# Optimization experiments

Hardware: AMD Instinct MI355X
Metric: run time of the kernel (lower is better)

## Reference

```python
import jax, jax.numpy as jnp
import numpy as np

B, H, W, C = 2, 256, 256, 96
NH, WS, SS = 3, 8, 4
HD = C // NH
N = WS * WS              # tokens per window
NWIMG = (H // WS) * (W // WS)  # windows per image
MLP = 4 * C
EPS = 1e-5

def _np_attn_mask():
    img = np.zeros((H, W))
    sl = (slice(0, -WS), slice(-WS, -SS), slice(-SS, None))
    cnt = 0
    for a in sl:
        for b in sl:
            img[a, b] = cnt
            cnt += 1
    m = img.reshape(H // WS, WS, W // WS, WS).transpose(0, 2, 1, 3).reshape(-1, N)
    am = m[:, None, :] - m[:, :, None]
    return np.where(am != 0, -100.0, 0.0).astype(np.float32)

def _np_rel_index():
    coords = np.stack(np.meshgrid(np.arange(WS), np.arange(WS), indexing='ij'))
    cf = coords.reshape(2, -1)
    rel = (cf[:, :, None] - cf[:, None, :]).transpose(1, 2, 0).copy()
    rel[..., 0] += WS - 1
    rel[..., 1] += WS - 1
    rel[..., 0] *= 2 * WS - 1
    return rel.sum(-1)

def _np_coords_table():
    r = np.arange(-(WS - 1), WS, dtype=np.float32)
    t = np.stack(np.meshgrid(r, r, indexing='ij'), axis=-1) / (WS - 1) * 8.0
    t = np.sign(t) * np.log2(np.abs(t) + 1.0) / np.log2(8.0)
    return t.reshape(-1, 2)

ATTN_MASK = jnp.asarray(_np_attn_mask())          # [NWIMG, N, N]
REL_INDEX = jnp.asarray(_np_rel_index().reshape(-1))
COORDS_TABLE = jnp.asarray(_np_coords_table())    # [(2WS-1)^2, 2]

def setup_inputs():
    key = jax.random.key(0)
    ks = jax.random.split(key, 16)
    s = 0.02
    return {
        'hidden_states': jax.random.normal(ks[0], (B, H * W, C), jnp.float32),
        'time': jax.random.uniform(ks[1], (B,), jnp.float32),
        'q_w': jax.random.normal(ks[2], (C, C), jnp.float32) * s,
        'q_b': jnp.zeros((C,), jnp.float32),
        'k_w': jax.random.normal(ks[3], (C, C), jnp.float32) * s,
        'v_w': jax.random.normal(ks[4], (C, C), jnp.float32) * s,
        'v_b': jnp.zeros((C,), jnp.float32),
        'proj_w': jax.random.normal(ks[5], (C, C), jnp.float32) * s,
        'proj_b': jnp.zeros((C,), jnp.float32),
        'logit_scale': jnp.full((NH, 1, 1), jnp.log(10.0), jnp.float32),
        'cpb_w1': jax.random.normal(ks[6], (2, 512), jnp.float32) * s,
        'cpb_b1': jnp.zeros((512,), jnp.float32),
        'cpb_w2': jax.random.normal(ks[7], (512, NH), jnp.float32) * s,
        'lnb_ww': jax.random.normal(ks[8], (1, C), jnp.float32) * s,
        'lnb_wb': jnp.ones((C,), jnp.float32),
        'lnb_bw': jax.random.normal(ks[9], (1, C), jnp.float32) * s,
        'lnb_bb': jnp.zeros((C,), jnp.float32),
        'lna_ww': jax.random.normal(ks[10], (1, C), jnp.float32) * s,
        'lna_wb': jnp.ones((C,), jnp.float32),
        'lna_bw': jax.random.normal(ks[11], (1, C), jnp.float32) * s,
        'lna_bb': jnp.zeros((C,), jnp.float32),
        'fc1_w': jax.random.normal(ks[12], (C, MLP), jnp.float32) * s,
        'fc1_b': jnp.zeros((MLP,), jnp.float32),
        'fc2_w': jax.random.normal(ks[13], (MLP, C), jnp.float32) * s,
        'fc2_b': jnp.zeros((C,), jnp.float32),
    }

def _cln(x, time, ww, wb, bw, bb):
    # ConditionalLayerNorm: stats over channels, affine params from time via Linear(1, C)
    mean = x.mean(-1, keepdims=True)
    var = (x * x).mean(-1, keepdims=True) - mean * mean
    xn = (x - mean) / jnp.sqrt(var + EPS)
    t = time.reshape(-1, 1)
    w = (t @ ww + wb)[:, None, :]
    b = (t @ bw + bb)[:, None, :]
    return w * xn + b

def reference(hidden_states, time, q_w, q_b, k_w, v_w, v_b, proj_w, proj_b, logit_scale, cpb_w1, cpb_b1, cpb_w2, lnb_ww, lnb_wb, lnb_bw, lnb_bb, lna_ww, lna_wb, lna_bw, lna_bb, fc1_w, fc1_b, fc2_w, fc2_b):
    shortcut = hidden_states
    x = hidden_states.reshape(B, H, W, C)
    x = jnp.roll(x, (-SS, -SS), axis=(1, 2))  # cyclic shift
    # window partition -> [nW, N, C]
    xw = x.reshape(B, H // WS, WS, W // WS, WS, C).transpose(0, 1, 3, 2, 4, 5).reshape(-1, N, C)
    nW = B * NWIMG
    q = (xw @ q_w + q_b).reshape(nW, N, NH, HD).transpose(0, 2, 1, 3)
    k = (xw @ k_w).reshape(nW, N, NH, HD).transpose(0, 2, 1, 3)  # key has no bias in Swinv2
    v = (xw @ v_w + v_b).reshape(nW, N, NH, HD).transpose(0, 2, 1, 3)
    # cosine attention with clamped learnable log temperature
    qn = q / jnp.maximum(jnp.linalg.norm(q, axis=-1, keepdims=True), 1e-12)
    kn = k / jnp.maximum(jnp.linalg.norm(k, axis=-1, keepdims=True), 1e-12)
    scale = jnp.exp(jnp.minimum(logit_scale, jnp.log(100.0)))  # [NH,1,1]
    attn = jnp.einsum('whnd,whmd->whnm', qn, kn) * scale[None]
    # continuous relative position bias: MLP(2->512->NH) over log-spaced coords
    bias_table = jax.nn.relu(COORDS_TABLE @ cpb_w1 + cpb_b1) @ cpb_w2
    bias = bias_table[REL_INDEX].reshape(N, N, NH).transpose(2, 0, 1)
    attn = attn + 16.0 * jax.nn.sigmoid(bias)[None]
    # shifted-window mask
    attn = attn.reshape(B, NWIMG, NH, N, N) + ATTN_MASK[None, :, None]
    attn = jax.nn.softmax(attn.reshape(nW, NH, N, N), axis=-1)
    ctx = jnp.einsum('whnm,whmd->whnd', attn, v).transpose(0, 2, 1, 3).reshape(nW, N, C)
    ctx = ctx @ proj_w + proj_b
    # window reverse + un-shift
    xr = ctx.reshape(B, H // WS, W // WS, WS, WS, C).transpose(0, 1, 3, 2, 4, 5).reshape(B, H, W, C)
    xr = jnp.roll(xr, (SS, SS), axis=(1, 2))
    attn_out = xr.reshape(B, H * W, C)
    # post-norm residual (Swin v2 style) with conditional LN
    hs = shortcut + _cln(attn_out, time, lnb_ww, lnb_wb, lnb_bw, lnb_bb)
    inter = jax.nn.gelu(hs @ fc1_w + fc1_b, approximate=False)
    mlp_out = inter @ fc2_w + fc2_b
    return hs + _cln(mlp_out, time, lna_ww, lna_wb, lna_bw, lna_bb)
```

## Files before the change

### kernel.cpp

```cpp
#include <hip/hip_runtime.h>
#include <hip/hip_bf16.h>

typedef __bf16 bf16_t;
typedef bf16_t bf16x8 __attribute__((ext_vector_type(8)));
typedef bf16_t bf16x4 __attribute__((ext_vector_type(4)));
typedef float  f32x4  __attribute__((ext_vector_type(4)));

#define LDC 104
#define LDW 100
#define LDT 72
#define LDP 70

#define WS_WQ    0
#define WS_WK    19968
#define WS_WV    39936
#define WS_WP    59904
#define WS_FC1   79872
#define WS_FC2   156672
#define WS_BIAS  233472
#define WS_TBL   282624

__device__ __forceinline__ f32x4 mfma16(bf16x8 a, bf16x8 b, f32x4 c) {
    return __builtin_amdgcn_mfma_f32_16x16x32_bf16(a, b, c, 0, 0, 0);
}

__device__ __forceinline__ float cpbf(int v) {
    float x = (float)v * (8.0f / 7.0f);
    float l = log2f(fabsf(x) + 1.0f) * (1.0f / 3.0f);
    return x < 0.f ? -l : l;
}

__device__ __forceinline__ int regcnt(int t, int hw, int ww) {
    int r = t >> 3, c = t & 7;
    int rr = (hw == 31) ? (r < 4 ? 1 : 2) : 0;
    int cc = (ww == 31) ? (c < 4 ? 1 : 2) : 0;
    return rr * 3 + cc;
}

__global__ __launch_bounds__(256) void k0a_cpb(
    const float* __restrict__ cw1, const float* __restrict__ cb1,
    const float* __restrict__ cw2, char* __restrict__ ws)
{
    const int wv = threadIdx.x >> 6, lane = threadIdx.x & 63;
    const int e = blockIdx.x * 4 + wv;
    if (e >= 225) return;
    int ia = e / 15, ib = e % 15;
    float c0 = cpbf(ia - 7), c1 = cpbf(ib - 7);
    float a0 = 0.f, a1 = 0.f, a2 = 0.f;
    #pragma unroll
    for (int c = 0; c < 8; ++c) {
        int j = c * 64 + lane;
        float h = fmaf(c0, cw1[j], fmaf(c1, cw1[512 + j], cb1[j]));
        h = fmaxf(h, 0.f);
        a0 = fmaf(h, cw2[j * 3 + 0], a0);
        a1 = fmaf(h, cw2[j * 3 + 1], a1);
        a2 = fmaf(h, cw2[j * 3 + 2], a2);
    }
    #pragma unroll
    for (int m = 1; m < 64; m <<= 1) {
        a0 += __shfl_xor(a0, m);
        a1 += __shfl_xor(a1, m);
        a2 += __shfl_xor(a2, m);
    }
    if (lane == 0) {
        float* tbl = (float*)(ws + WS_TBL);
        tbl[e * 3 + 0] = a0; tbl[e * 3 + 1] = a1; tbl[e * 3 + 2] = a2;
    }
}

__global__ __launch_bounds__(512) void k0w_prep(
    const float* __restrict__ qw, const float* __restrict__ kw,
    const float* __restrict__ vw, const float* __restrict__ pw,
    const float* __restrict__ fc1w, const float* __restrict__ fc2w,
    char* __restrict__ ws)
{
    int tid = threadIdx.x;
    if (blockIdx.x < 54) {
        int rid = blockIdx.x * 512 + tid;
        if (rid < 9216) {
            int which = rid / 2304, r = rid % 2304;
            int i = r / 24, o4 = r % 24;
            const float* src = which == 0 ? qw : which == 1 ? kw : which == 2 ? vw : pw;
            float4 u = *(const float4*)(src + i * 96 + 4 * o4);
            bf16_t* dst = (bf16_t*)(ws + WS_WQ + which * 19968);
            dst[(4 * o4 + 0) * LDC + i] = (bf16_t)u.x;
            dst[(4 * o4 + 1) * LDC + i] = (bf16_t)u.y;
            dst[(4 * o4 + 2) * LDC + i] = (bf16_t)u.z;
            dst[(4 * o4 + 3) * LDC + i] = (bf16_t)u.w;
        } else if (rid < 18432) {
            int r = rid - 9216;
            int i = r / 96, m4 = r % 96;
            float4 u = *(const float4*)(fc1w + i * 384 + 4 * m4);
            bf16_t* dst = (bf16_t*)(ws + WS_FC1);
            dst[(4 * m4 + 0) * LDW + i] = (bf16_t)u.x;
            dst[(4 * m4 + 1) * LDW + i] = (bf16_t)u.y;
            dst[(4 * m4 + 2) * LDW + i] = (bf16_t)u.z;
            dst[(4 * m4 + 3) * LDW + i] = (bf16_t)u.w;
        } else {
            int r = rid - 18432;
            int g = r / 24, o4 = r % 24;
            int ch = g / 96, m = g % 96;
            float4 u = *(const float4*)(fc2w + g * 96 + 4 * o4);
            bf16_t* dst = (bf16_t*)(ws + WS_FC2);
            dst[(ch * 96 + 4 * o4 + 0) * LDW + m] = (bf16_t)u.x;
            dst[(ch * 96 + 4 * o4 + 1) * LDW + m] = (bf16_t)u.y;
            dst[(ch * 96 + 4 * o4 + 2) * LDW + m] = (bf16_t)u.z;
            dst[(ch * 96 + 4 * o4 + 3) * LDW + m] = (bf16_t)u.w;
        }
    } else {
        int e = (blockIdx.x - 54) * 512 + tid;
        if (e < 12288) {
            const float* tbl = (const float*)(ws + WS_TBL);
            float* bias = (float*)(ws + WS_BIAS);
            int h = e >> 12, nm = e & 4095, n = nm >> 6, m = nm & 63;
            int dr = (n >> 3) - (m >> 3) + 7, dc = (n & 7) - (m & 7) + 7;
            float t = tbl[(dr * 15 + dc) * 3 + h];
            bias[(h << 12) | (n << 6) | ((m & 15) << 2) | (m >> 4)] = 16.f / (1.f + __expf(-t));
        }
    }
}

__global__ __launch_bounds__(256, 3) void kA_attn(
    const float* __restrict__ hidden, const float* __restrict__ tv,
    const float* __restrict__ qb, const float* __restrict__ vb,
    const float* __restrict__ pb, const float* __restrict__ lsc,
    const float* __restrict__ lnww, const float* __restrict__ lnwb,
    const float* __restrict__ lnbw, const float* __restrict__ lnbb,
    const char* __restrict__ ws, float* __restrict__ hs)
{
    __shared__ __align__(16) char sm[40704];
    bf16_t* vT   = (bf16_t*)(sm + 0);
    bf16_t* qn   = (bf16_t*)(sm + 13824);
    bf16_t* kn   = (bf16_t*)(sm + 27136);
    bf16_t* P    = (bf16_t*)(sm + 13824);
    bf16_t* ctxb = (bf16_t*)(sm + 0);

    const int tid = threadIdx.x;
    const int wv = tid >> 6, lane = tid & 63, lg = lane >> 4, lr = lane & 15;
    const int wid = blockIdx.x;
    const int bat = wid >> 10, wim = wid & 1023, hw = wim >> 5, wwi = wim & 31;

    {
        bf16x8 af[3];
        {
            int tok = 16 * wv + lr;
            int gr = ((hw << 3) + (tok >> 3) + 4) & 255;
            int gc = ((wwi << 3) + (tok & 7) + 4) & 255;
            const float* xb = hidden + (((size_t)bat << 16) + (gr << 8) + gc) * 96;
            #pragma unroll
            for (int ks = 0; ks < 3; ++ks) {
                float4 u0 = *(const float4*)(xb + 32 * ks + 8 * lg);
                float4 u1 = *(const float4*)(xb + 32 * ks + 8 * lg + 4);
                bf16x8 f;
                f[0] = (bf16_t)u0.x; f[1] = (bf16_t)u0.y; f[2] = (bf16_t)u0.z; f[3] = (bf16_t)u0.w;
                f[4] = (bf16_t)u1.x; f[5] = (bf16_t)u1.y; f[6] = (bf16_t)u1.z; f[7] = (bf16_t)u1.w;
                af[ks] = f;
            }
        }
        const bf16_t* Wq = (const bf16_t*)(ws + WS_WQ);
        const bf16_t* Wk = (const bf16_t*)(ws + WS_WK);
        const bf16_t* Wv = (const bf16_t*)(ws + WS_WV);

        {
            bf16x8 wf[6][3];
            #pragma unroll
            for (int n = 0; n < 6; ++n)
                #pragma unroll
                for (int ks = 0; ks < 3; ++ks)
                    wf[n][ks] = *(const bf16x8*)(Wq + (16 * n + lr) * LDC + 32 * ks + 8 * lg);
            f32x4 acc[6];
            #pragma unroll
            for (int n = 0; n < 6; ++n) {
                f32x4 a = {0.f,0.f,0.f,0.f};
                #pragma unroll
                for (int ks = 0; ks < 3; ++ks) a = mfma16(af[ks], wf[n][ks], a);
                float bq = qb[16 * n + lr];
                #pragma unroll
                for (int j = 0; j < 4; ++j) a[j] += bq;
                acc[n] = a;
            }
            #pragma unroll
            for (int h = 0; h < 3; ++h)
                #pragma unroll
                for (int j = 0; j < 4; ++j) {
                    float s = acc[2*h][j] * acc[2*h][j] + acc[2*h+1][j] * acc[2*h+1][j];
                    s += __shfl_xor(s, 1); s += __shfl_xor(s, 2); s += __shfl_xor(s, 4); s += __shfl_xor(s, 8);
                    float inv = 1.f / fmaxf(sqrtf(s), 1e-12f);
                    int row = 16 * wv + 4 * lg + j;
                    qn[row * LDC + 32 * h + lr]      = (bf16_t)(acc[2*h][j] * inv);
                    qn[row * LDC + 32 * h + 16 + lr] = (bf16_t)(acc[2*h+1][j] * inv);
                }
        }
        {
            bf16x8 wf[6][3];
            #pragma unroll
            for (int n = 0; n < 6; ++n)
                #pragma unroll
                for (int ks = 0; ks < 3; ++ks)
                    wf[n][ks] = *(const bf16x8*)(Wk + (16 * n + lr) * LDC + 32 * ks + 8 * lg);
            f32x4 acc[6];
            #pragma unroll
            for (int n = 0; n < 6; ++n) {
                f32x4 a = {0.f,0.f,0.f,0.f};
                #pragma unroll
                for (int ks = 0; ks < 3; ++ks) a = mfma16(af[ks], wf[n][ks], a);
                acc[n] = a;
            }
            #pragma unroll
            for (int h = 0; h < 3; ++h)
                #pragma unroll
                for (int j = 0; j < 4; ++j) {
                    float s = acc[2*h][j] * acc[2*h][j] + acc[2*h+1][j] * acc[2*h+1][j];
                    s += __shfl_xor(s, 1); s += __shfl_xor(s, 2); s += __shfl_xor(s, 4); s += __shfl_xor(s, 8);
                    float inv = 1.f / fmaxf(sqrtf(s), 1e-12f);
                    int row = 16 * wv + 4 * lg + j;
                    kn[row * LDC + 32 * h + lr]      = (bf16_t)(acc[2*h][j] * inv);
                    kn[row * LDC + 32 * h + 16 + lr] = (bf16_t)(acc[2*h+1][j] * inv);
                }
        }
        {
            bf16x8 wf[6][3];
            #pragma unroll
            for (int n = 0; n < 6; ++n)
                #pragma unroll
                for (int ks = 0; ks < 3; ++ks)
                    wf[n][ks] = *(const bf16x8*)(Wv + (16 * n + lr) * LDC + 32 * ks + 8 * lg);
            #pragma unroll
            for (int n = 0; n < 6; ++n) {
                f32x4 a = {0.f,0.f,0.f,0.f};
                #pragma unroll
                for (int ks = 0; ks < 3; ++ks) a = mfma16(af[ks], wf[n][ks], a);
                float bv_ = vb[16 * n + lr];
                bf16x4 pk;
                #pragma unroll
                for (int j = 0; j < 4; ++j) pk[j] = (bf16_t)(a[j] + bv_);
                *(bf16x4*)(vT + (16 * n + lr) * LDT + 16 * wv + 4 * lg) = pk;
            }
        }
    }
    __syncthreads();

    {
        float br[3][4][4];
        const float* biasT = (const float*)(ws + WS_BIAS);
        #pragma unroll
        for (int h = 0; h < 3; ++h)
            #pragma unroll
            for (int j = 0; j < 4; ++j) {
                float4 u = *(const float4*)(biasT + (h << 12) + ((16 * wv + 4 * lg + j) << 6) + (lr << 2));
                br[h][0][j] = u.x; br[h][1][j] = u.y; br[h][2][j] = u.z; br[h][3][j] = u.w;
            }

        f32x4 s[3][4];
        #pragma unroll
        for (int h = 0; h < 3; ++h) {
            bf16x8 aq = *(const bf16x8*)(qn + (16 * wv + lr) * LDC + 32 * h + 8 * lg);
            bf16x8 bk[4];
            #pragma unroll
            for (int f = 0; f < 4; ++f)
                bk[f] = *(const bf16x8*)(kn + (16 * f + lr) * LDC + 32 * h + 8 * lg);
            #pragma unroll
            for (int f = 0; f < 4; ++f) {
                f32x4 z = {0.f,0.f,0.f,0.f};
                s[h][f] = mfma16(aq, bk[f], z);
            }
        }
        __syncthreads();

        float ls[3];
        #pragma unroll
        for (int h = 0; h < 3; ++h) ls[h] = __expf(fminf(lsc[h], 4.6051702f));
        int cntm[4], cnti[4];
        #pragma unroll
        for (int f = 0; f < 4; ++f) cntm[f] = regcnt(16 * f + lr, hw, wwi);
        #pragma unroll
        for (int j = 0; j < 4; ++j) cnti[j] = regcnt(16 * wv + 4 * lg + j, hw, wwi);
        #pragma unroll
        for (int h = 0; h < 3; ++h) {
            #pragma unroll
            for (int f = 0; f < 4; ++f)
                #pragma unroll
                for (int j = 0; j < 4; ++j) {
                    float mk = (cnti[j] != cntm[f]) ? -100.f : 0.f;
                    s[h][f][j] = fmaf(s[h][f][j], ls[h], br[h][f][j] + mk);
                }
            #pragma unroll
            for (int j = 0; j < 4; ++j) {
                float mx = fmaxf(fmaxf(s[h][0][j], s[h][1][j]), fmaxf(s[h][2][j], s[h][3][j]));
                mx = fmaxf(mx, __shfl_xor(mx, 1)); mx = fmaxf(mx, __shfl_xor(mx, 2));
                mx = fmaxf(mx, __shfl_xor(mx, 4)); mx = fmaxf(mx, __shfl_xor(mx, 8));
                float sum = 0.f;
                #pragma unroll
                for (int f = 0; f < 4; ++f) { float e = __expf(s[h][f][j] - mx); s[h][f][j] = e; sum += e; }
                sum += __shfl_xor(sum, 1); sum += __shfl_xor(sum, 2); sum += __shfl_xor(sum, 4); sum += __shfl_xor(sum, 8);
                float inv = 1.f / sum;
                int row = 16 * wv + 4 * lg + j;
                #pragma unroll
                for (int f = 0; f < 4; ++f)
                    P[h * 64 * LDP + row * LDP + 16 * f + lr] = (bf16_t)(s[h][f][j] * inv);
            }
        }
    }
    __syncthreads();

    {
        f32x4 ctx[6];
        #pragma unroll
        for (int t = 0; t < 6; ++t) { f32x4 z = {0.f,0.f,0.f,0.f}; ctx[t] = z; }
        bf16x8 ap[3][2], bv2[3][2][2];
        #pragma unroll
        for (int h = 0; h < 3; ++h)
            #pragma unroll
            for (int ks = 0; ks < 2; ++ks) {
                ap[h][ks] = *(const bf16x8*)(P + h * 64 * LDP + (16 * wv + lr) * LDP + 32 * ks + 8 * lg);
                #pragma unroll
                for (int dt = 0; dt < 2; ++dt)
                    bv2[h][dt][ks] = *(const bf16x8*)(vT + (32 * h + 16 * dt + lr) * LDT + 32 * ks + 8 * lg);
            }
        #pragma unroll
        for (int h = 0; h < 3; ++h)
            #pragma unroll
            for (int ks = 0; ks < 2; ++ks)
                #pragma unroll
                for (int dt = 0; dt < 2; ++dt)
                    ctx[2 * h + dt] = mfma16(ap[h][ks], bv2[h][dt][ks], ctx[2 * h + dt]);
        __syncthreads();
        #pragma unroll
        for (int t = 0; t < 6; ++t)
            #pragma unroll
            for (int j = 0; j < 4; ++j)
                ctxb[(16 * wv + 4 * lg + j) * LDC + 16 * t + lr] = (bf16_t)ctx[t][j];
    }
    __syncthreads();

    {
        const bf16_t* Wp = (const bf16_t*)(ws + WS_WP);
        bf16x8 wf[6][3];
        #pragma unroll
        for (int n = 0; n < 6; ++n)
            #pragma unroll
            for (int ks = 0; ks < 3; ++ks)
                wf[n][ks] = *(const bf16x8*)(Wp + (16 * n + lr) * LDC + 32 * ks + 8 * lg);
        bf16x8 af[3];
        #pragma unroll
        for (int ks = 0; ks < 3; ++ks) af[ks] = *(const bf16x8*)(ctxb + (16 * wv + lr) * LDC + 32 * ks + 8 * lg);
        f32x4 acc[6];
        #pragma unroll
        for (int n = 0; n < 6; ++n) {
            f32x4 a = {0.f,0.f,0.f,0.f};
            #pragma unroll
            for (int ks = 0; ks < 3; ++ks) a = mfma16(af[ks], wf[n][ks], a);
            float bp = pb[16 * n + lr];
            #pragma unroll
            for (int j = 0; j < 4; ++j) a[j] += bp;
            acc[n] = a;
        }
        float tb = tv[bat];
        float wco[6], bco[6];
        #pragma unroll
        for (int t = 0; t < 6; ++t) {
            int col = 16 * t + lr;
            wco[t] = fmaf(tb, lnww[col], lnwb[col]);
            bco[t] = fmaf(tb, lnbw[col], lnbb[col]);
        }
        #pragma unroll
        for (int j = 0; j < 4; ++j) {
            float smn = 0.f, sq = 0.f;
            #pragma unroll
            for (int t = 0; t < 6; ++t) { float v = acc[t][j]; smn += v; sq = fmaf(v, v, sq); }
            smn += __shfl_xor(smn, 1); smn += __shfl_xor(smn, 2); smn += __shfl_xor(smn, 4); smn += __shfl_xor(smn, 8);
            sq  += __shfl_xor(sq, 1);  sq  += __shfl_xor(sq, 2);  sq  += __shfl_xor(sq, 4);  sq  += __shfl_xor(sq, 8);
            float mean = smn * (1.f / 96.f);
            float var  = sq * (1.f / 96.f) - mean * mean;
            float rstd = rsqrtf(var + 1e-5f);
            int trow = 16 * wv + 4 * lg + j;
            int gr = ((hw << 3) + (trow >> 3) + 4) & 255;
            int gc = ((wwi << 3) + (trow & 7) + 4) & 255;
            size_t gbase = (((size_t)bat << 16) + (gr << 8) + gc) * 96;
            float hid[6];
            #pragma unroll
            for (int t = 0; t < 6; ++t) hid[t] = hidden[gbase + 16 * t + lr];
            #pragma unroll
            for (int t = 0; t < 6; ++t) {
                float xn = (acc[t][j] - mean) * rstd;
                hs[gbase + 16 * t + lr] = hid[t] + fmaf(wco[t], xn, bco[t]);
            }
        }
    }
}

__global__ __launch_bounds__(256, 2) void kB_mlp(
    const float* __restrict__ tv, const float* __restrict__ fc1b,
    const float* __restrict__ fc2b,
    const float* __restrict__ lnww, const float* __restrict__ lnwb,
    const float* __restrict__ lnbw, const float* __restrict__ lnbb,
    const char* __restrict__ ws, float* __restrict__ io)
{
    __shared__ __align__(16) char smem[65024];
    bf16_t* w1c  = (bf16_t*)(smem + 0);
    bf16_t* w2c  = (bf16_t*)(smem + 19200);
    bf16_t* gbuf = (bf16_t*)(smem + 38400);

    const int tid = threadIdx.x;
    const int wv = tid >> 6, lane = tid & 63, lg = lane >> 4, lr = lane & 15;
    const int tblk = blockIdx.x * 128;
    const float tb = tv[tblk >> 16];

    bf16x8 af[2][3];
    #pragma unroll
    for (int mt = 0; mt < 2; ++mt) {
        const float* hb = io + (size_t)(tblk + 32 * wv + 16 * mt + lr) * 96;
        #pragma unroll
        for (int ks = 0; ks < 3; ++ks) {
            float4 u0 = *(const float4*)(hb + 32 * ks + 8 * lg);
            float4 u1 = *(const float4*)(hb + 32 * ks + 8 * lg + 4);
            bf16x8 f;
            f[0] = (bf16_t)u0.x; f[1] = (bf16_t)u0.y; f[2] = (bf16_t)u0.z; f[3] = (bf16_t)u0.w;
            f[4] = (bf16_t)u1.x; f[5] = (bf16_t)u1.y; f[6] = (bf16_t)u1.z; f[7] = (bf16_t)u1.w;
            af[mt][ks] = f;
        }
    }

    f32x4 mlp[2][6];
    #pragma unroll
    for (int mt = 0; mt < 2; ++mt)
        #pragma unroll
        for (int ot = 0; ot < 6; ++ot) { f32x4 z = {0.f,0.f,0.f,0.f}; mlp[mt][ot] = z; }

    #pragma unroll 1
    for (int ch = 0; ch < 4; ++ch) {
        if (ch) __syncthreads();
        {
            const float4* s1 = (const float4*)(ws + WS_FC1 + ch * 19200);
            const float4* s2 = (const float4*)(ws + WS_FC2 + ch * 19200);
            float4* d1 = (float4*)w1c;
            float4* d2 = (float4*)w2c;
            #pragma unroll
            for (int i = 0; i < 5; ++i) {
                int idx = tid + 256 * i;
                if (idx < 1200) { d1[idx] = s1[idx]; d2[idx] = s2[idx]; }
            }
        }
        __syncthreads();

        #pragma unroll
        for (int nt = 0; nt < 6; ++nt) {
            bf16x8 b1[3];
            #pragma unroll
            for (int ks = 0; ks < 3; ++ks)
                b1[ks] = *(const bf16x8*)(w1c + (16 * nt + lr) * LDW + 32 * ks + 8 * lg);
            float bb = fc1b[96 * ch + 16 * nt + lr];
            #pragma unroll
            for (int mt = 0; mt < 2; ++mt) {
                f32x4 a = {0.f,0.f,0.f,0.f};
                #pragma unroll
                for (int ks = 0; ks < 3; ++ks) a = mfma16(af[mt][ks], b1[ks], a);
                #pragma unroll
                for (int j = 0; j < 4; ++j) {
                    float x = a[j] + bb;
                    float u = 0.7978845608f * fmaf(0.044715f * x, x * x, x);
                    float t = __expf(2.f * u);
                    float g = x - x * __builtin_amdgcn_rcpf(t + 1.f);
                    gbuf[(32 * wv + 16 * mt + 4 * lg + j) * LDC + 16 * nt + lr] = (bf16_t)g;
                }
            }
        }
        __syncthreads();

        #pragma unroll
        for (int kk = 0; kk < 3; ++kk) {
            bf16x8 gf[2];
            #pragma unroll
            for (int mt = 0; mt < 2; ++mt)
                gf[mt] = *(const bf16x8*)(gbuf + (32 * wv + 16 * mt + lr) * LDC + 32 * kk + 8 * lg);
            #pragma unroll
            for (int oh = 0; oh < 2; ++oh) {
                bf16x8 a2[3];
                #pragma unroll
                for (int o3 = 0; o3 < 3; ++o3)
                    a2[o3] = *(const bf16x8*)(w2c + (16 * (3 * oh + o3) + lr) * LDW + 32 * kk + 8 * lg);
                #pragma unroll
                for (int mt = 0; mt < 2; ++mt)
                    #pragma unroll
                    for (int o3 = 0; o3 < 3; ++o3)
                        mlp[mt][3 * oh + o3] = mfma16(gf[mt], a2[o3], mlp[mt][3 * oh + o3]);
            }
        }
    }

    float wco[6], bco[6];
    #pragma unroll
    for (int ot = 0; ot < 6; ++ot) {
        int col = 16 * ot + lr;
        wco[ot] = fmaf(tb, lnww[col], lnwb[col]);
        bco[ot] = fmaf(tb, lnbw[col], lnbb[col]);
    }
    #pragma unroll
    for (int mt = 0; mt < 2; ++mt) {
        #pragma unroll
        for (int ot = 0; ot < 6; ++ot) {
            float bb = fc2b[16 * ot + lr];
            #pragma unroll
            for (int j = 0; j < 4; ++j) mlp[mt][ot][j] += bb;
        }
        #pragma unroll
        for (int j = 0; j < 4; ++j) {
            float smn = 0.f, sq = 0.f;
            #pragma unroll
            for (int ot = 0; ot < 6; ++ot) { float v = mlp[mt][ot][j]; smn += v; sq = fmaf(v, v, sq); }
            smn += __shfl_xor(smn, 1); smn += __shfl_xor(smn, 2); smn += __shfl_xor(smn, 4); smn += __shfl_xor(smn, 8);
            sq  += __shfl_xor(sq, 1);  sq  += __shfl_xor(sq, 2);  sq  += __shfl_xor(sq, 4);  sq  += __shfl_xor(sq, 8);
            float mean = smn * (1.f / 96.f);
            float var  = sq * (1.f / 96.f) - mean * mean;
            float rstd = rsqrtf(var + 1e-5f);
            size_t row = (size_t)tblk + 32 * wv + 16 * mt + 4 * lg + j;
            float hid[6];
            #pragma unroll
            for (int ot = 0; ot < 6; ++ot) hid[ot] = io[row * 96 + 16 * ot + lr];
            #pragma unroll
            for (int ot = 0; ot < 6; ++ot) {
                float xn = (mlp[mt][ot][j] - mean) * rstd;
                io[row * 96 + 16 * ot + lr] = hid[ot] + fmaf(wco[ot], xn, bco[ot]);
            }
        }
    }
}

extern "C" void kernel_launch(void* const* d_in, const int* in_sizes, int n_in,
                              void* d_out, int out_size, void* d_ws, size_t ws_size,
                              hipStream_t stream)
{
    const float* hidden = (const float*)d_in[0];
    const float* tv     = (const float*)d_in[1];
    const float* q_w    = (const float*)d_in[2];
    const float* q_b    = (const float*)d_in[3];
    const float* k_w    = (const float*)d_in[4];
    const float* v_w    = (const float*)d_in[5];
    const float* v_b    = (const float*)d_in[6];
    const float* p_w    = (const float*)d_in[7];
    const float* p_b    = (const float*)d_in[8];
    const float* lsc    = (const float*)d_in[9];
    const float* cw1    = (const float*)d_in[10];
    const float* cb1    = (const float*)d_in[11];
    const float* cw2    = (const float*)d_in[12];
    const float* lnb_ww = (const float*)d_in[13];
    const float* lnb_wb = (const float*)d_in[14];
    const float* lnb_bw = (const float*)d_in[15];
    const float* lnb_bb = (const float*)d_in[16];
    const float* lna_ww = (const float*)d_in[17];
    const float* lna_wb = (const float*)d_in[18];
    const float* lna_bw = (const float*)d_in[19];
    const float* lna_bb = (const float*)d_in[20];
    const float* fc1_w  = (const float*)d_in[21];
    const float* fc1_b  = (const float*)d_in[22];
    const float* fc2_w  = (const float*)d_in[23];
    const float* fc2_b  = (const float*)d_in[24];
    char* ws = (char*)d_ws;
    float* out = (float*)d_out;

    k0a_cpb<<<dim3(57), dim3(256), 0, stream>>>(cw1, cb1, cw2, ws);
    k0w_prep<<<dim3(78), dim3(512), 0, stream>>>(q_w, k_w, v_w, p_w, fc1_w, fc2_w, ws);
    kA_attn<<<dim3(2048), dim3(256), 0, stream>>>(hidden, tv, q_b, v_b, p_b, lsc,
                                                  lnb_ww, lnb_wb, lnb_bw, lnb_bb, ws, out);
    kB_mlp<<<dim3(1024), dim3(256), 0, stream>>>(tv, fc1_b, fc2_b,
                                                 lna_ww, lna_wb, lna_bw, lna_bb, ws, out);
}
```

Measured before the change: 293.3 us.

## Fuse MLP stage into attention kernel to keep hidden state on chip

```diff
diff --git a/kernel.cpp b/kernel.cpp
--- a/kernel.cpp
+++ b/kernel.cpp
@@ -120,13 +120,16 @@
     }
 }
 
-__global__ __launch_bounds__(256, 3) void kA_attn(
+__global__ __launch_bounds__(256, 3) void kAB(
     const float* __restrict__ hidden, const float* __restrict__ tv,
     const float* __restrict__ qb, const float* __restrict__ vb,
     const float* __restrict__ pb, const float* __restrict__ lsc,
-    const float* __restrict__ lnww, const float* __restrict__ lnwb,
-    const float* __restrict__ lnbw, const float* __restrict__ lnbb,
-    const char* __restrict__ ws, float* __restrict__ hs)
+    const float* __restrict__ lnbww, const float* __restrict__ lnbwb,
+    const float* __restrict__ lnbbw, const float* __restrict__ lnbbb,
+    const float* __restrict__ lnaww, const float* __restrict__ lnawb,
+    const float* __restrict__ lnabw, const float* __restrict__ lnabb,
+    const float* __restrict__ fc1b, const float* __restrict__ fc2b,
+    const char* __restrict__ ws, float* __restrict__ out)
 {
     __shared__ __align__(16) char sm[40704];
     bf16_t* vT   = (bf16_t*)(sm + 0);
@@ -134,6 +137,8 @@
     bf16_t* kn   = (bf16_t*)(sm + 27136);
     bf16_t* P    = (bf16_t*)(sm + 13824);
     bf16_t* ctxb = (bf16_t*)(sm + 0);
+    bf16_t* gbuf = (bf16_t*)(sm + 13824);
+    bf16_t* hsb  = (bf16_t*)(sm + 27136);
 
     const int tid = threadIdx.x;
     const int wv = tid >> 6, lane = tid & 63, lg = lane >> 4, lr = lane & 15;
@@ -333,14 +338,9 @@
     }
     __syncthreads();
 
+    float hsr[6][4];
     {
         const bf16_t* Wp = (const bf16_t*)(ws + WS_WP);
-        bf16x8 wf[6][3];
-        #pragma unroll
-        for (int n = 0; n < 6; ++n)
-            #pragma unroll
-            for (int ks = 0; ks < 3; ++ks)
-                wf[n][ks] = *(const bf16x8*)(Wp + (16 * n + lr) * LDC + 32 * ks + 8 * lg);
         bf16x8 af[3];
         #pragma unroll
         for (int ks = 0; ks < 3; ++ks) af[ks] = *(const bf16x8*)(ctxb + (16 * wv + lr) * LDC + 32 * ks + 8 * lg);
@@ -349,7 +349,8 @@
         for (int n = 0; n < 6; ++n) {
             f32x4 a = {0.f,0.f,0.f,0.f};
             #pragma unroll
-            for (int ks = 0; ks < 3; ++ks) a = mfma16(af[ks], wf[n][ks], a);
+            for (int ks = 0; ks < 3; ++ks)
+                a = mfma16(af[ks], *(const bf16x8*)(Wp + (16 * n + lr) * LDC + 32 * ks + 8 * lg), a);
             float bp = pb[16 * n + lr];
             #pragma unroll
             for (int j = 0; j < 4; ++j) a[j] += bp;
@@ -360,8 +361,8 @@
         #pragma unroll
         for (int t = 0; t < 6; ++t) {
             int col = 16 * t + lr;
-            wco[t] = fmaf(tb, lnww[col], lnwb[col]);
-            bco[t] = fmaf(tb, lnbw[col], lnbb[col]);
+            wco[t] = fmaf(tb, lnbww[col], lnbwb[col]);
+            bco[t] = fmaf(tb, lnbbw[col], lnbbb[col]);
         }
         #pragma unroll
         for (int j = 0; j < 4; ++j) {
@@ -383,144 +384,87 @@
             #pragma unroll
             for (int t = 0; t < 6; ++t) {
                 float xn = (acc[t][j] - mean) * rstd;
-                hs[gbase + 16 * t + lr] = hid[t] + fmaf(wco[t], xn, bco[t]);
-            }
-        }
-    }
-}
-
-__global__ __launch_bounds__(256, 2) void kB_mlp(
-    const float* __restrict__ tv, const float* __restrict__ fc1b,
-    const float* __restrict__ fc2b,
-    const float* __restrict__ lnww, const float* __restrict__ lnwb,
-    const float* __restrict__ lnbw, const float* __restrict__ lnbb,
-    const char* __restrict__ ws, float* __restrict__ io)
-{
-    __shared__ __align__(16) char smem[65024];
-    bf16_t* w1c  = (bf16_t*)(smem + 0);
-    bf16_t* w2c  = (bf16_t*)(smem + 19200);
-    bf16_t* gbuf = (bf16_t*)(smem + 38400);
-
-    const int tid = threadIdx.x;
-    const int wv = tid >> 6, lane = tid & 63, lg = lane >> 4, lr = lane & 15;
-    const int tblk = blockIdx.x * 128;
-    const float tb = tv[tblk >> 16];
-
-    bf16x8 af[2][3];
-    #pragma unroll
-    for (int mt = 0; mt < 2; ++mt) {
-        const float* hb = io + (size_t)(tblk + 32 * wv + 16 * mt + lr) * 96;
-        #pragma unroll
-        for (int ks = 0; ks < 3; ++ks) {
-            float4 u0 = *(const float4*)(hb + 32 * ks + 8 * lg);
-            float4 u1 = *(const float4*)(hb + 32 * ks + 8 * lg + 4);
-            bf16x8 f;
-            f[0] = (bf16_t)u0.x; f[1] = (bf16_t)u0.y; f[2] = (bf16_t)u0.z; f[3] = (bf16_t)u0.w;
-            f[4] = (bf16_t)u1.x; f[5] = (bf16_t)u1.y; f[6] = (bf16_t)u1.z; f[7] = (bf16_t)u1.w;
-            af[mt][ks] = f;
-        }
-    }
-
-    f32x4 mlp[2][6];
-    #pragma unroll
-    for (int mt = 0; mt < 2; ++mt)
-        #pragma unroll
-        for (int ot = 0; ot < 6; ++ot) { f32x4 z = {0.f,0.f,0.f,0.f}; mlp[mt][ot] = z; }
-
-    #pragma unroll 1
-    for (int ch = 0; ch < 4; ++ch) {
-        if (ch) __syncthreads();
-        {
-            const float4* s1 = (const float4*)(ws + WS_FC1 + ch * 19200);
-            const float4* s2 = (const float4*)(ws + WS_FC2 + ch * 19200);
-            float4* d1 = (float4*)w1c;
-            float4* d2 = (float4*)w2c;
-            #pragma unroll
-            for (int i = 0; i < 5; ++i) {
-                int idx = tid + 256 * i;
-                if (idx < 1200) { d1[idx] = s1[idx]; d2[idx] = s2[idx]; }
-            }
-        }
-        __syncthreads();
-
-        #pragma unroll
-        for (int nt = 0; nt < 6; ++nt) {
-            bf16x8 b1[3];
-            #pragma unroll
-            for (int ks = 0; ks < 3; ++ks)
-                b1[ks] = *(const bf16x8*)(w1c + (16 * nt + lr) * LDW + 32 * ks + 8 * lg);
-            float bb = fc1b[96 * ch + 16 * nt + lr];
-            #pragma unroll
-            for (int mt = 0; mt < 2; ++mt) {
+                float hsv = hid[t] + fmaf(wco[t], xn, bco[t]);
+                hsr[t][j] = hsv;
+                hsb[trow * LDC + 16 * t + lr] = (bf16_t)hsv;
+            }
+        }
+    }
+
+    f32x4 mlp[6];
+    {
+        const bf16_t* w1 = (const bf16_t*)(ws + WS_FC1);
+        const bf16_t* w2 = (const bf16_t*)(ws + WS_FC2);
+        bf16x8 af2[3];
+        #pragma unroll
+        for (int ks = 0; ks < 3; ++ks)
+            af2[ks] = *(const bf16x8*)(hsb + (16 * wv + lr) * LDC + 32 * ks + 8 * lg);
+        #pragma unroll
+        for (int t = 0; t < 6; ++t) { f32x4 z = {0.f,0.f,0.f,0.f}; mlp[t] = z; }
+
+        #pragma unroll 1
+        for (int ch = 0; ch < 4; ++ch) {
+            #pragma unroll
+            for (int nt = 0; nt < 6; ++nt) {
+                bf16x8 b1[3];
+                #pragma unroll
+                for (int ks = 0; ks < 3; ++ks)
+                    b1[ks] = *(const bf16x8*)(w1 + (96 * ch + 16 * nt + lr) * LDW + 32 * ks + 8 * lg);
                 f32x4 a = {0.f,0.f,0.f,0.f};
                 #pragma unroll
-                for (int ks = 0; ks < 3; ++ks) a = mfma16(af[mt][ks], b1[ks], a);
+                for (int ks = 0; ks < 3; ++ks) a = mfma16(af2[ks], b1[ks], a);
+                float bb = fc1b[96 * ch + 16 * nt + lr];
                 #pragma unroll
                 for (int j = 0; j < 4; ++j) {
                     float x = a[j] + bb;
                     float u = 0.7978845608f * fmaf(0.044715f * x, x * x, x);
-                    float t = __expf(2.f * u);
-                    float g = x - x * __builtin_amdgcn_rcpf(t + 1.f);
-                    gbuf[(32 * wv + 16 * mt + 4 * lg + j) * LDC + 16 * nt + lr] = (bf16_t)g;
+                    float t2 = __expf(2.f * u);
+                    float g = x - x * __builtin_amdgcn_rcpf(t2 + 1.f);
+                    gbuf[(16 * wv + 4 * lg + j) * LDC + 16 * nt + lr] = (bf16_t)g;
                 }
             }
-        }
-        __syncthreads();
-
-        #pragma unroll
-        for (int kk = 0; kk < 3; ++kk) {
-            bf16x8 gf[2];
-            #pragma unroll
-            for (int mt = 0; mt < 2; ++mt)
-                gf[mt] = *(const bf16x8*)(gbuf + (32 * wv + 16 * mt + lr) * LDC + 32 * kk + 8 * lg);
-            #pragma unroll
-            for (int oh = 0; oh < 2; ++oh) {
-                bf16x8 a2[3];
-                #pragma unroll
-                for (int o3 = 0; o3 < 3; ++o3)
-                    a2[o3] = *(const bf16x8*)(w2c + (16 * (3 * oh + o3) + lr) * LDW + 32 * kk + 8 * lg);
-                #pragma unroll
-                for (int mt = 0; mt < 2; ++mt)
-                    #pragma unroll
-                    for (int o3 = 0; o3 < 3; ++o3)
-                        mlp[mt][3 * oh + o3] = mfma16(gf[mt], a2[o3], mlp[mt][3 * oh + o3]);
-            }
-        }
-    }
-
-    float wco[6], bco[6];
-    #pragma unroll
-    for (int ot = 0; ot < 6; ++ot) {
-        int col = 16 * ot + lr;
-        wco[ot] = fmaf(tb, lnww[col], lnwb[col]);
-        bco[ot] = fmaf(tb, lnbw[col], lnbb[col]);
-    }
-    #pragma unroll
-    for (int mt = 0; mt < 2; ++mt) {
-        #pragma unroll
-        for (int ot = 0; ot < 6; ++ot) {
-            float bb = fc2b[16 * ot + lr];
-            #pragma unroll
-            for (int j = 0; j < 4; ++j) mlp[mt][ot][j] += bb;
+            #pragma unroll
+            for (int kk = 0; kk < 3; ++kk) {
+                bf16x8 gf = *(const bf16x8*)(gbuf + (16 * wv + lr) * LDC + 32 * kk + 8 * lg);
+                #pragma unroll
+                for (int n = 0; n < 6; ++n) {
+                    bf16x8 a2 = *(const bf16x8*)(w2 + (96 * ch + 16 * n + lr) * LDW + 32 * kk + 8 * lg);
+                    mlp[n] = mfma16(gf, a2, mlp[n]);
+                }
+            }
+        }
+    }
+
+    {
+        float tb = tv[bat];
+        float wco[6], bco[6];
+        #pragma unroll
+        for (int t = 0; t < 6; ++t) {
+            int col = 16 * t + lr;
+            wco[t] = fmaf(tb, lnaww[col], lnawb[col]);
+            bco[t] = fmaf(tb, lnabw[col], lnabb[col]);
+            float bb = fc2b[col];
+            #pragma unroll
+            for (int j = 0; j < 4; ++j) mlp[t][j] += bb;
         }
         #pragma unroll
         for (int j = 0; j < 4; ++j) {
             float smn = 0.f, sq = 0.f;
             #pragma unroll
-            for (int ot = 0; ot < 6; ++ot) { float v = mlp[mt][ot][j]; smn += v; sq = fmaf(v, v, sq); }
+            for (int t = 0; t < 6; ++t) { float v = mlp[t][j]; smn += v; sq = fmaf(v, v, sq); }
             smn += __shfl_xor(smn, 1); smn += __shfl_xor(smn, 2); smn += __shfl_xor(smn, 4); smn += __shfl_xor(smn, 8);
             sq  += __shfl_xor(sq, 1);  sq  += __shfl_xor(sq, 2);  sq  += __shfl_xor(sq, 4);  sq  += __shfl_xor(sq, 8);
             float mean = smn * (1.f / 96.f);
             float var  = sq * (1.f / 96.f) - mean * mean;
             float rstd = rsqrtf(var + 1e-5f);
-            size_t row = (size_t)tblk + 32 * wv + 16 * mt + 4 * lg + j;
-            float hid[6];
-            #pragma unroll
-            for (int ot = 0; ot < 6; ++ot) hid[ot] = io[row * 96 + 16 * ot + lr];
-            #pragma unroll
-            for (int ot = 0; ot < 6; ++ot) {
-                float xn = (mlp[mt][ot][j] - mean) * rstd;
-                io[row * 96 + 16 * ot + lr] = hid[ot] + fmaf(wco[ot], xn, bco[ot]);
+            int trow = 16 * wv + 4 * lg + j;
+            int gr = ((hw << 3) + (trow >> 3) + 4) & 255;
+            int gc = ((wwi << 3) + (trow & 7) + 4) & 255;
+            size_t gbase = (((size_t)bat << 16) + (gr << 8) + gc) * 96;
+            #pragma unroll
+            for (int t = 0; t < 6; ++t) {
+                float xn = (mlp[t][j] - mean) * rstd;
+                out[gbase + 16 * t + lr] = hsr[t][j] + fmaf(wco[t], xn, bco[t]);
             }
         }
     }
@@ -560,8 +504,8 @@
 
     k0a_cpb<<<dim3(57), dim3(256), 0, stream>>>(cw1, cb1, cw2, ws);
     k0w_prep<<<dim3(78), dim3(512), 0, stream>>>(q_w, k_w, v_w, p_w, fc1_w, fc2_w, ws);
-    kA_attn<<<dim3(2048), dim3(256), 0, stream>>>(hidden, tv, q_b, v_b, p_b, lsc,
-                                                  lnb_ww, lnb_wb, lnb_bw, lnb_bb, ws, out);
-    kB_mlp<<<dim3(1024), dim3(256), 0, stream>>>(tv, fc1_b, fc2_b,
-                                                 lna_ww, lna_wb, lna_bw, lna_bb, ws, out);
-}
+    kAB<<<dim3(2048), dim3(256), 0, stream>>>(hidden, tv, q_b, v_b, p_b, lsc,
+                                              lnb_ww, lnb_wb, lnb_bw, lnb_bb,
+                                              lna_ww, lna_wb, lna_bw, lna_bb,
+                                              fc1_b, fc2_b, ws, out);
+}
```

Result: faster. 270.3 us (-7.8%).
